# Optimization experiments

Measured on AMD Instinct MI355X. Metric: run time of the kernel, lower is better.

Reference implementation:

```python
import jax, jax.numpy as jnp
import numpy as np

N, E, FIN, H, F = 50000, 800000, 256, 8, 32


def setup_inputs() -> dict:
    key = jax.random.key(0)
    ks = jax.random.split(key, 7)
    x = jax.random.normal(ks[0], (N, FIN), dtype=jnp.float32)
    edge_index = jax.random.randint(ks[1], (2, E), 0, N, dtype=jnp.int64)
    # Glorot-ish scaled params
    W = jax.random.normal(ks[2], (FIN, H * F), dtype=jnp.float32) * (1.0 / np.sqrt(FIN))
    a_src = jax.random.normal(ks[3], (H, F), dtype=jnp.float32) * 0.1
    a_trg = jax.random.normal(ks[4], (H, F), dtype=jnp.float32) * 0.1
    skip_W = jax.random.normal(ks[5], (FIN, H * F), dtype=jnp.float32) * (1.0 / np.sqrt(FIN))
    bias = jnp.zeros((H * F,), dtype=jnp.float32)
    return {"x": x, "edge_index": edge_index, "W": W, "a_src": a_src,
            "a_trg": a_trg, "skip_W": skip_W, "bias": bias}


def reference(x, edge_index, W, a_src, a_trg, skip_W, bias):
    num_nodes = x.shape[0]
    src, trg = edge_index[0], edge_index[1]

    # linear projection  (N, H, F)
    proj = (x @ W).reshape(num_nodes, H, F)

    # per-node attention logits  (N, H)
    scores_source = jnp.einsum('nhf,hf->nh', proj, a_src)
    scores_target = jnp.einsum('nhf,hf->nh', proj, a_trg)

    # lift to edges and score  (E, H)
    scores_per_edge = jax.nn.leaky_relu(scores_source[src] + scores_target[trg],
                                        negative_slope=0.2)
    # global-max subtraction (as in original), then segment softmax over target
    scores_per_edge = scores_per_edge - jnp.max(scores_per_edge)
    exp_scores = jnp.exp(scores_per_edge)
    denom = jax.ops.segment_sum(exp_scores, trg, num_segments=num_nodes)  # (N, H)
    att = exp_scores / (denom[trg] + 1e-16)  # (E, H)

    # weighted aggregation  (N, H, F)
    weighted = proj[src] * att[:, :, None]
    out = jax.ops.segment_sum(weighted, trg, num_segments=num_nodes)

    # skip connection (F != FIN -> projected skip)
    out = out + (x @ skip_W).reshape(num_nodes, H, F)

    # concat heads + bias + ELU
    out = out.reshape(num_nodes, H * F) + bias
    return jax.nn.elu(out)
```

## Files before the change

kernel.cpp:

```cpp
#include <hip/hip_runtime.h>
#include <hip/hip_bf16.h>

#define FIN   256
#define HF    256
#define NCOL  512
#define HEADS 8
#define FDIM  32
#define L2E   1.44269504f
#define BCAP  64
#define NBB   256

typedef float f32x4 __attribute__((ext_vector_type(4)));
typedef __bf16 bf16x8 __attribute__((ext_vector_type(8)));
typedef unsigned short u16x8 __attribute__((ext_vector_type(8)));

__device__ __forceinline__ unsigned short f2bf(float f) {
  unsigned u = __float_as_uint(f);
  u = u + 0x7FFFu + ((u >> 16) & 1u);
  return (unsigned short)(u >> 16);
}
__device__ __forceinline__ float bf2f(unsigned short s) {
  return __uint_as_float(((unsigned)s) << 16);
}
__device__ __forceinline__ unsigned cvt_pk_bf16(float a, float b) {
  unsigned r;
  asm("v_cvt_pk_bf16_f32 %0, %1, %2" : "=v"(r) : "v"(a), "v"(b));
  return r;
}
__device__ __forceinline__ void gload_lds16(const unsigned short* g, unsigned short* l) {
  __builtin_amdgcn_global_load_lds(
      (const __attribute__((address_space(1))) void*)g,
      (__attribute__((address_space(3))) void*)l,
      16, 0, 0);
}

__global__ void k_prep(const float* __restrict__ W, const float* __restrict__ SW,
                       unsigned short* __restrict__ WT) {
  int tid = blockIdx.x * 256 + threadIdx.x;
  int c = tid >> 8, k = tid & 255;
  float v = (c < HF) ? W[(size_t)k * HF + c] : SW[(size_t)k * HF + (c - HF)];
  WT[(size_t)c * FIN + k] = f2bf(v);
}

__global__ __launch_bounds__(512, 2) void k_gemm(const float* __restrict__ X,
                                                 const unsigned short* __restrict__ WT,
                                                 const float* __restrict__ a_src,
                                                 const float* __restrict__ a_trg,
                                                 unsigned short* __restrict__ Pb,
                                                 float* __restrict__ ss,
                                                 float* __restrict__ st, int Nn,
                                                 const int* __restrict__ eidx,
                                                 int* __restrict__ cnt,
                                                 int* __restrict__ bucket,
                                                 int E, int gblocks) {
  __shared__ __align__(16) unsigned short As[128 * 32];
  __shared__ __align__(16) unsigned short Bs[512 * 32];
  if (blockIdx.x >= gblocks) {
    for (int e = (blockIdx.x - gblocks) * 512 + threadIdx.x; e < E; e += NBB * 512) {
      int trg = eidx[E + e];
      int pos = atomicAdd(&cnt[trg], 1);
      if (pos < BCAP) bucket[((unsigned)trg << 6) + pos] = eidx[e];
    }
    return;
  }
  const int t = threadIdx.x;
  const int bm0 = blockIdx.x * 128;
  const int lane = t & 63, wid = t >> 6;
  const int wm = wid >> 2, wn = wid & 3;
  const int lo = lane & 15, g = lane >> 4;
  const int swz = (lo >> 2) & 3;
  f32x4 acc[4][8];
#pragma unroll
  for (int i = 0; i < 4; ++i)
#pragma unroll
    for (int j = 0; j < 8; ++j) acc[i][j] = (f32x4){0.f, 0.f, 0.f, 0.f};

  const int arow = t >> 2, aseg0 = t & 3;
  const int aq = aseg0 ^ ((t >> 4) & 3);
  int grow = bm0 + arow; if (grow > Nn - 1) grow = Nn - 1;
  const float* xsrc = X + (size_t)grow * FIN + aseg0 * 8;
  unsigned short* adst = As + arow * 32 + aq * 8;
  const int bcol = lane >> 2;
  const int bseg = (lane & 3) ^ ((lane >> 4) & 3);

  float4 f0 = *(const float4*)(xsrc);
  float4 f1 = *(const float4*)(xsrc + 4);

  for (int kk = 0; kk < FIN; kk += 32) {
#pragma unroll
    for (int j = 0; j < 4; ++j) {
      int cg = wid * 4 + j;
      const unsigned short* gp =
          WT + (size_t)(cg * 16 + bcol) * FIN + kk + bseg * 8;
      gload_lds16(gp, Bs + cg * 512);
    }
    uint4 ap = {cvt_pk_bf16(f0.x, f0.y), cvt_pk_bf16(f0.z, f0.w),
                cvt_pk_bf16(f1.x, f1.y), cvt_pk_bf16(f1.z, f1.w)};
    *(uint4*)adst = ap;
    if (kk + 32 < FIN) {
      f0 = *(const float4*)(xsrc + kk + 32);
      f1 = *(const float4*)(xsrc + kk + 36);
    }
    __syncthreads();
    bf16x8 a[4], b[8];
#pragma unroll
    for (int mi = 0; mi < 4; ++mi)
      a[mi] = __builtin_bit_cast(bf16x8,
          *(const u16x8*)(As + (wm * 64 + mi * 16 + lo) * 32 + ((g ^ swz) * 8)));
#pragma unroll
    for (int ni = 0; ni < 8; ++ni)
      b[ni] = __builtin_bit_cast(bf16x8,
          *(const u16x8*)(Bs + (wn * 128 + ni * 16 + lo) * 32 + ((g ^ swz) * 8)));
#pragma unroll
    for (int mi = 0; mi < 4; ++mi)
#pragma unroll
      for (int ni = 0; ni < 8; ++ni)
        acc[mi][ni] = __builtin_amdgcn_mfma_f32_16x16x32_bf16(b[ni], a[mi], acc[mi][ni], 0, 0, 0);
    __syncthreads();
  }
#pragma unroll
  for (int mi = 0; mi < 4; ++mi) {
    int gr = bm0 + wm * 64 + mi * 16 + lo;
    if (gr < Nn) {
#pragma unroll
      for (int ni = 0; ni < 8; ++ni) {
        f32x4 v = acc[mi][ni];
        uint2 pk = {cvt_pk_bf16(v[0], v[1]), cvt_pk_bf16(v[2], v[3])};
        *(uint2*)(Pb + (size_t)gr * NCOL + wn * 128 + ni * 16 + g * 4) = pk;
      }
    }
  }
  if (wn < 2) {
    float psS[4][4], psT[4][4];
#pragma unroll
    for (int mi = 0; mi < 4; ++mi)
#pragma unroll
      for (int hd = 0; hd < 4; ++hd) { psS[mi][hd] = 0.f; psT[mi][hd] = 0.f; }
    const int cbase = wn * 128 + g * 4;
#pragma unroll
    for (int ni = 0; ni < 8; ++ni) {
      float4 av = *(const float4*)(a_src + cbase + ni * 16);
      float4 tv = *(const float4*)(a_trg + cbase + ni * 16);
      int hd = ni >> 1;
#pragma unroll
      for (int mi = 0; mi < 4; ++mi) {
        f32x4 v = acc[mi][ni];
        psS[mi][hd] += v[0]*av.x + v[1]*av.y + v[2]*av.z + v[3]*av.w;
        psT[mi][hd] += v[0]*tv.x + v[1]*tv.y + v[2]*tv.z + v[3]*tv.w;
      }
    }
#pragma unroll
    for (int mi = 0; mi < 4; ++mi) {
      int gr = bm0 + wm * 64 + mi * 16 + lo;
#pragma unroll
      for (int hd = 0; hd < 4; ++hd) {
        float s = psS[mi][hd]; s += __shfl_xor(s, 16); s += __shfl_xor(s, 32);
        float tt = psT[mi][hd]; tt += __shfl_xor(tt, 16); tt += __shfl_xor(tt, 32);
        if (g == hd && gr < Nn) {
          ss[(size_t)gr * 8 + wn * 4 + hd] = s * L2E;
          st[(size_t)gr * 8 + wn * 4 + hd] = tt * L2E;
        }
      }
    }
  }
}

__global__ __launch_bounds__(256) void k_agg(const unsigned short* __restrict__ Pb,
    const int* __restrict__ cnt, const int* __restrict__ bucket,
    const float* __restrict__ ss, const float* __restrict__ st,
    const float* __restrict__ bias, float* __restrict__ out, int Nn) {
  int n = blockIdx.x * 4 + (threadIdx.x >> 6);
  if (n >= Nn) return;
  const int l = threadIdx.x & 63;
  const int h = l >> 3;
  const float sth = st[(unsigned)n * 8 + h];
  float a0 = 0.f, a1 = 0.f, a2 = 0.f, a3 = 0.f, dsum = 0.f;
  int cn = cnt[n]; if (cn > BCAP) cn = BCAP;
  const int* bk = bucket + ((unsigned)n << 6);
  int i = 0;
  for (; i + 1 < cn; i += 2) {
    int s0 = bk[i], s1 = bk[i + 1];
    float v0 = ss[((unsigned)s0 << 3) + h];
    float v1 = ss[((unsigned)s1 << 3) + h];
    ushort4 p0 = *(const ushort4*)(Pb + ((unsigned)s0 << 9) + (l << 2));
    ushort4 p1 = *(const ushort4*)(Pb + ((unsigned)s1 << 9) + (l << 2));
    float x0 = v0 + sth; x0 = fmaxf(x0, 0.2f * x0);
    float x1 = v1 + sth; x1 = fmaxf(x1, 0.2f * x1);
    float w0 = __builtin_amdgcn_exp2f(x0);
    float w1 = __builtin_amdgcn_exp2f(x1);
    dsum += w0 + w1;
    a0 += w0 * bf2f(p0.x) + w1 * bf2f(p1.x);
    a1 += w0 * bf2f(p0.y) + w1 * bf2f(p1.y);
    a2 += w0 * bf2f(p0.z) + w1 * bf2f(p1.z);
    a3 += w0 * bf2f(p0.w) + w1 * bf2f(p1.w);
  }
  if (i < cn) {
    int s0 = bk[i];
    float v0 = ss[((unsigned)s0 << 3) + h];
    ushort4 p0 = *(const ushort4*)(Pb + ((unsigned)s0 << 9) + (l << 2));
    float x0 = v0 + sth; x0 = fmaxf(x0, 0.2f * x0);
    float w0 = __builtin_amdgcn_exp2f(x0);
    dsum += w0;
    a0 += w0 * bf2f(p0.x); a1 += w0 * bf2f(p0.y);
    a2 += w0 * bf2f(p0.z); a3 += w0 * bf2f(p0.w);
  }
  float inv = 1.f / (dsum + 1e-16f);
  ushort4 sk = *(const ushort4*)(Pb + ((unsigned)n << 9) + HF + (l << 2));
  float4 bi = *(const float4*)(bias + (l << 2));
  float o0 = a0 * inv + bf2f(sk.x) + bi.x;
  float o1 = a1 * inv + bf2f(sk.y) + bi.y;
  float o2 = a2 * inv + bf2f(sk.z) + bi.z;
  float o3 = a3 * inv + bf2f(sk.w) + bi.w;
  o0 = o0 > 0.f ? o0 : expm1f(o0);
  o1 = o1 > 0.f ? o1 : expm1f(o1);
  o2 = o2 > 0.f ? o2 : expm1f(o2);
  o3 = o3 > 0.f ? o3 : expm1f(o3);
  float4 o = {o0, o1, o2, o3};
  *(float4*)(out + ((unsigned)n << 8) + (l << 2)) = o;
}

extern "C" void kernel_launch(void* const* d_in, const int* in_sizes, int n_in,
                              void* d_out, int out_size, void* d_ws, size_t ws_size,
                              hipStream_t stream) {
  const float* x      = (const float*)d_in[0];
  const int*   eidx   = (const int*)d_in[1];
  const float* W      = (const float*)d_in[2];
  const float* a_src  = (const float*)d_in[3];
  const float* a_trg  = (const float*)d_in[4];
  const float* skip_W = (const float*)d_in[5];
  const float* bias   = (const float*)d_in[6];
  float* out = (float*)d_out;
  const int Nn = in_sizes[0] / FIN;
  const int E  = in_sizes[1] / 2;

  char* p = (char*)d_ws;
  auto carve = [&](size_t bytes) { char* r = p; p += (bytes + 255) & ~(size_t)255; return r; };
  unsigned short* WT = (unsigned short*)carve((size_t)NCOL * FIN * 2);
  unsigned short* Pb = (unsigned short*)carve((size_t)Nn * NCOL * 2);
  float* ss   = (float*)carve((size_t)Nn * HEADS * 4);
  float* st   = (float*)carve((size_t)Nn * HEADS * 4);
  int* cnt    = (int*)carve((size_t)Nn * 4);
  int* bucket = (int*)carve((size_t)Nn * BCAP * 4);

  hipMemsetAsync(cnt, 0, (size_t)Nn * 4, stream);

  hipLaunchKernelGGL(k_prep, dim3((NCOL * FIN) / 256), dim3(256), 0, stream,
                     W, skip_W, WT);
  const int gblocks = (Nn + 127) / 128;
  hipLaunchKernelGGL(k_gemm, dim3(gblocks + NBB), dim3(512), 0, stream,
                     x, WT, a_src, a_trg, Pb, ss, st, Nn,
                     eidx, cnt, bucket, E, gblocks);
  hipLaunchKernelGGL(k_agg, dim3((Nn + 3) / 4), dim3(256), 0, stream,
                     Pb, cnt, bucket, ss, st, bias, out, Nn);
}
```

Measured before the change: 153.6 us.

## Stage full A tile in LDS once and read weights directly from global

The GEMM kernel now converts the whole 128x256 X tile to bf16 into LDS with an XOR swizzle in a single pass, then runs the K loop with no per-iteration barriers. B fragments are loaded straight from global memory (L2-cached WT) instead of being staged through LDS via global_load_lds. This removes the eight per-step barrier pairs and the B staging, at the cost of 64KB of LDS per block, which may cut occupancy below the two blocks per CU the launch bounds ask for, and of uncoalesced global B reads on the critical path.

Result: slower. 160.7 us (+4.6%).

```diff
diff --git a/kernel.cpp b/kernel.cpp
--- a/kernel.cpp
+++ b/kernel.cpp
@@ -26,12 +26,6 @@
   unsigned r;
   asm("v_cvt_pk_bf16_f32 %0, %1, %2" : "=v"(r) : "v"(a), "v"(b));
   return r;
-}
-__device__ __forceinline__ void gload_lds16(const unsigned short* g, unsigned short* l) {
-  __builtin_amdgcn_global_load_lds(
-      (const __attribute__((address_space(1))) void*)g,
-      (__attribute__((address_space(3))) void*)l,
-      16, 0, 0);
 }
 
 __global__ void k_prep(const float* __restrict__ W, const float* __restrict__ SW,
@@ -53,8 +47,7 @@
                                                  int* __restrict__ cnt,
                                                  int* __restrict__ bucket,
                                                  int E, int gblocks) {
-  __shared__ __align__(16) unsigned short As[128 * 32];
-  __shared__ __align__(16) unsigned short Bs[512 * 32];
+  __shared__ __align__(16) unsigned short As[128 * FIN];
   if (blockIdx.x >= gblocks) {
     for (int e = (blockIdx.x - gblocks) * 512 + threadIdx.x; e < E; e += NBB * 512) {
       int trg = eidx[E + e];
@@ -68,55 +61,51 @@
   const int lane = t & 63, wid = t >> 6;
   const int wm = wid >> 2, wn = wid & 3;
   const int lo = lane & 15, g = lane >> 4;
-  const int swz = (lo >> 2) & 3;
+  const int rsw = lo & 7;
   f32x4 acc[4][8];
 #pragma unroll
   for (int i = 0; i < 4; ++i)
 #pragma unroll
     for (int j = 0; j < 8; ++j) acc[i][j] = (f32x4){0.f, 0.f, 0.f, 0.f};
 
-  const int arow = t >> 2, aseg0 = t & 3;
-  const int aq = aseg0 ^ ((t >> 4) & 3);
-  int grow = bm0 + arow; if (grow > Nn - 1) grow = Nn - 1;
-  const float* xsrc = X + (size_t)grow * FIN + aseg0 * 8;
-  unsigned short* adst = As + arow * 32 + aq * 8;
-  const int bcol = lane >> 2;
-  const int bseg = (lane & 3) ^ ((lane >> 4) & 3);
-
-  float4 f0 = *(const float4*)(xsrc);
-  float4 f1 = *(const float4*)(xsrc + 4);
-
+  {
+    const int r = t >> 2, s = t & 3;
+    int gr = bm0 + r; if (gr > Nn - 1) gr = Nn - 1;
+    const float* xp = X + (size_t)gr * FIN + s * 64;
+    unsigned short* ap = As + r * FIN;
+    const int rx = r & 7;
+#pragma unroll
+    for (int q = 0; q < 8; ++q) {
+      float4 u0 = *(const float4*)(xp + q * 8);
+      float4 u1 = *(const float4*)(xp + q * 8 + 4);
+      uint4 pk = {cvt_pk_bf16(u0.x, u0.y), cvt_pk_bf16(u0.z, u0.w),
+                  cvt_pk_bf16(u1.x, u1.y), cvt_pk_bf16(u1.z, u1.w)};
+      int qq = (s * 8 + q) ^ rx;
+      *(uint4*)(ap + qq * 8) = pk;
+    }
+  }
+  __syncthreads();
+
+  const unsigned short* wb = WT + (size_t)(wn * 128) * FIN;
+#pragma unroll
   for (int kk = 0; kk < FIN; kk += 32) {
-#pragma unroll
-    for (int j = 0; j < 4; ++j) {
-      int cg = wid * 4 + j;
-      const unsigned short* gp =
-          WT + (size_t)(cg * 16 + bcol) * FIN + kk + bseg * 8;
-      gload_lds16(gp, Bs + cg * 512);
-    }
-    uint4 ap = {cvt_pk_bf16(f0.x, f0.y), cvt_pk_bf16(f0.z, f0.w),
-                cvt_pk_bf16(f1.x, f1.y), cvt_pk_bf16(f1.z, f1.w)};
-    *(uint4*)adst = ap;
-    if (kk + 32 < FIN) {
-      f0 = *(const float4*)(xsrc + kk + 32);
-      f1 = *(const float4*)(xsrc + kk + 36);
-    }
-    __syncthreads();
-    bf16x8 a[4], b[8];
-#pragma unroll
-    for (int mi = 0; mi < 4; ++mi)
-      a[mi] = __builtin_bit_cast(bf16x8,
-          *(const u16x8*)(As + (wm * 64 + mi * 16 + lo) * 32 + ((g ^ swz) * 8)));
+    bf16x8 b[8], a[4];
 #pragma unroll
     for (int ni = 0; ni < 8; ++ni)
       b[ni] = __builtin_bit_cast(bf16x8,
-          *(const u16x8*)(Bs + (wn * 128 + ni * 16 + lo) * 32 + ((g ^ swz) * 8)));
+          *(const u16x8*)(wb + (size_t)(ni * 16 + lo) * FIN + kk + g * 8));
+#pragma unroll
+    for (int mi = 0; mi < 4; ++mi) {
+      int row = wm * 64 + mi * 16 + lo;
+      int qa = (kk >> 3) + g;
+      a[mi] = __builtin_bit_cast(bf16x8,
+          *(const u16x8*)(As + row * FIN + ((qa ^ rsw) * 8)));
+    }
 #pragma unroll
     for (int mi = 0; mi < 4; ++mi)
 #pragma unroll
       for (int ni = 0; ni < 8; ++ni)
         acc[mi][ni] = __builtin_amdgcn_mfma_f32_16x16x32_bf16(b[ni], a[mi], acc[mi][ni], 0, 0, 0);
-    __syncthreads();
   }
 #pragma unroll
   for (int mi = 0; mi < 4; ++mi) {
```
